# Optimization experiments

Measured on AMD Instinct MI355X. Metric: run time of the kernel, lower is better.

The kernel has to match this reference:

```python
import jax, jax.numpy as jnp
import numpy as np

NEG = -1e9      # stands in for -inf; exp(NEG)=0 in fp32 and is grad-safe
SK_TAU = 0.05   # sinkhorn temperature (module constant)


def _gconv(A, x, Wa, ba, Wu, bu):
    # Gconv: A <- F.normalize(A, p=1, dim=-2) (column-wise L1), then
    # out = A @ relu(a_fc(x)) + relu(u_fc(x))
    Anorm = A / jnp.maximum(jnp.sum(jnp.abs(A), axis=1, keepdims=True), 1e-12)
    ax = jax.nn.relu(x @ Wa + ba)
    ux = jax.nn.relu(x @ Wu + bu)
    return jnp.einsum('bnm,bmd->bnd', Anorm, ax) + ux


def _sinkhorn(s, n1, n2, max_iter, tau):
    # Masked, batched equivalent of the per-sample torch sinkhorn
    # (valid region [0:n1, 0:n2]; entries outside stay at NEG -> exp -> 0).
    # Assumes n1 <= n2 == N so no per-sample transpose branch triggers.
    B, N, M = s.shape
    row_ok = jnp.arange(N)[None, :, None] < n1[:, None, None]
    col_ok = jnp.arange(M)[None, None, :] < n2[:, None, None]
    mask = row_ok & col_ok
    log_s = jnp.where(mask, s / tau, NEG)
    for i in range(max_iter):
        axis = 2 if i % 2 == 0 else 1  # even: row-normalize, odd: col-normalize
        log_s = log_s - jax.scipy.special.logsumexp(log_s, axis=axis, keepdims=True)
        log_s = jnp.where(mask, log_s, NEG)
    return jnp.exp(log_s)


def _forward(feat1, feat2, A1, A2, n1, n2, sk_max_iter,
             W0a, b0a, W0u, b0u, W1a, b1a, W1u, b1u, Wc, bc, Aaff0, Aaff1):
    # gnn layer 0 (Siamese: same weights on both graphs)
    emb1 = _gconv(A1, feat1, W0a, b0a, W0u, b0u)
    emb2 = _gconv(A2, feat2, W0a, b0a, W0u, b0u)
    # i == gnn_layer-2: affinity -> sinkhorn -> cross-graph update
    s = jnp.einsum('bnd,de,bme->bnm', emb1, Aaff0, emb2)
    s = _sinkhorn(s, n1, n2, sk_max_iter, SK_TAU)
    new1 = jnp.concatenate([emb1, jnp.einsum('bnm,bmd->bnd', s, emb2)], axis=-1) @ Wc + bc
    new2 = jnp.concatenate([emb2, jnp.einsum('bnm,bnd->bmd', s, emb1)], axis=-1) @ Wc + bc
    emb1, emb2 = new1, new2
    # gnn layer 1 (final)
    emb1 = _gconv(A1, emb1, W1a, b1a, W1u, b1u)
    emb2 = _gconv(A2, emb2, W1a, b1a, W1u, b1u)
    s = jnp.einsum('bnd,de,bme->bnm', emb1, Aaff1, emb2)
    return _sinkhorn(s, n1, n2, sk_max_iter, SK_TAU)


def setup_inputs() -> dict:
    key = jax.random.key(0)
    B, N = 32, 256
    C_IN, C_HID, C_OUT = 1024, 2048, 2048
    ks = jax.random.split(key, 16)

    feat1 = jax.random.normal(ks[0], (B, N, C_IN), dtype=jnp.float32)
    feat2 = jax.random.normal(ks[1], (B, N, C_IN), dtype=jnp.float32)
    A1 = jax.random.uniform(ks[2], (B, N, N), dtype=jnp.float32)
    A2 = jax.random.uniform(ks[3], (B, N, N), dtype=jnp.float32)
    n1 = jax.random.randint(ks[4], (B,), N // 2, N + 1).astype(jnp.int32)
    n2 = jnp.full((B,), N, dtype=jnp.int32)

    def lin(k, fan_in, fan_out):
        stdv = 1.0 / np.sqrt(fan_in)
        kw, kb = jax.random.split(k)
        W = jax.random.uniform(kw, (fan_in, fan_out), minval=-stdv, maxval=stdv, dtype=jnp.float32)
        b = jax.random.uniform(kb, (fan_out,), minval=-stdv, maxval=stdv, dtype=jnp.float32)
        return W, b

    W0a, b0a = lin(ks[5], C_IN, C_HID)
    W0u, b0u = lin(ks[6], C_IN, C_HID)
    W1a, b1a = lin(ks[7], C_HID, C_OUT)
    W1u, b1u = lin(ks[8], C_HID, C_OUT)
    Wc, bc = lin(ks[9], 2 * C_HID, C_HID)
    # WeightedInnerProdAffinity: A ~ U(-1/sqrt(d), 1/sqrt(d)) + I
    Aaff0 = jax.random.uniform(ks[10], (C_HID, C_HID), minval=-1/np.sqrt(C_HID), maxval=1/np.sqrt(C_HID), dtype=jnp.float32) + jnp.eye(C_HID, dtype=jnp.float32)
    Aaff1 = jax.random.uniform(ks[11], (C_OUT, C_OUT), minval=-1/np.sqrt(C_OUT), maxval=1/np.sqrt(C_OUT), dtype=jnp.float32) + jnp.eye(C_OUT, dtype=jnp.float32)

    return {
        'feat1': feat1, 'feat2': feat2, 'A1': A1, 'A2': A2,
        'n1': n1, 'n2': n2, 'cross_iter_num': -1, 'sk_max_iter': 10,
        'W0a': W0a, 'b0a': b0a, 'W0u': W0u, 'b0u': b0u,
        'W1a': W1a, 'b1a': b1a, 'W1u': W1u, 'b1u': b1u,
        'Wc': Wc, 'bc': bc, 'Aaff0': Aaff0, 'Aaff1': Aaff1,
    }


def reference(feat1, feat2, A1, A2, n1, n2, cross_iter_num, sk_max_iter,
              W0a, b0a, W0u, b0u, W1a, b1a, W1u, b1u, Wc, bc, Aaff0, Aaff1):
    assert cross_iter_num <= 0  # PCA-GM path (IPCA-GM cross-iteration not exercised)
    return _forward(feat1, feat2, A1, A2, n1, n2, int(sk_max_iter),
                    W0a, b0a, W0u, b0u, W1a, b1a, W1u, b1u, Wc, bc, Aaff0, Aaff1)
```

## Files before the change

### kernel.cpp

```cpp
#include <hip/hip_runtime.h>
#include <math.h>

#define NEGV -1e9f
#define SK_TAU 0.05f

typedef __attribute__((ext_vector_type(4))) float f32x4;
typedef __attribute__((ext_vector_type(8))) short short8;

#define GLDS(g, l) __builtin_amdgcn_global_load_lds( \
    (const __attribute__((address_space(1))) void*)(g), \
    (__attribute__((address_space(3))) void*)(l), 16, 0, 0)

__device__ inline unsigned bf16rtn(float x) {
    unsigned u = __float_as_uint(x);
    return (u + 0x7FFFu + ((u >> 16) & 1u)) >> 16;
}
__device__ inline float bf2f(short h) {
    return __uint_as_float(((unsigned)(unsigned short)h) << 16);
}
__device__ inline void split1(float x, short& h, short& l) {
    unsigned hu = bf16rtn(x);
    h = (short)hu;
    float r = x - __uint_as_float(hu << 16);
    l = (short)(__float_as_uint(r) >> 16);
}
__device__ inline void cvt4(const float4 v, short4& h, short4& l) {
    unsigned h0 = bf16rtn(v.x), h1 = bf16rtn(v.y), h2 = bf16rtn(v.z), h3 = bf16rtn(v.w);
    h.x = (short)h0; h.y = (short)h1; h.z = (short)h2; h.w = (short)h3;
    float l0 = v.x - __uint_as_float(h0 << 16);
    float l1 = v.y - __uint_as_float(h1 << 16);
    float l2 = v.z - __uint_as_float(h2 << 16);
    float l3 = v.w - __uint_as_float(h3 << 16);
    l.x = (short)(__float_as_uint(l0) >> 16);
    l.y = (short)(__float_as_uint(l1) >> 16);
    l.z = (short)(__float_as_uint(l2) >> 16);
    l.w = (short)(__float_as_uint(l3) >> 16);
}
__device__ inline short8 pack8(const short4 a, const short4 b) {
    short8 r;
    r[0] = a.x; r[1] = a.y; r[2] = a.z; r[3] = a.w;
    r[4] = b.x; r[5] = b.y; r[6] = b.z; r[7] = b.w;
    return r;
}

__global__ __launch_bounds__(256) void colnorm_k(const float* __restrict__ A,
                                                 float* __restrict__ inv)
{
    int idx = blockIdx.x * 256 + threadIdx.x;
    int b = idx >> 8, m = idx & 255;
    const float* p = A + (long long)b * 65536 + m;
    float s = 0.f;
    #pragma unroll 8
    for (int n = 0; n < 256; ++n) s += fabsf(p[n * 256]);
    inv[idx] = 1.f / fmaxf(s, 1e-12f);
}

__global__ __launch_bounds__(256) void split_mat(const float* __restrict__ X,
                                                 short* __restrict__ H,
                                                 short* __restrict__ L, long long n4)
{
    long long i = (long long)blockIdx.x * 256 + threadIdx.x;
    long long stride = (long long)gridDim.x * 256;
    for (; i < n4; i += stride) {
        float4 v = ((const float4*)X)[i];
        short4 h, l;
        cvt4(v, h, l);
        ((short4*)H)[i] = h;
        ((short4*)L)[i] = l;
    }
}

template <int OM>
__global__ __launch_bounds__(256, 2) void gemm_w(
    const short* __restrict__ A1h, const short* __restrict__ A1l,
    const short* __restrict__ A2h, const short* __restrict__ A2l,
    int K1, int lda,
    const float* __restrict__ Bf, int K,
    float* __restrict__ Cf, short* __restrict__ Ch, short* __restrict__ Cl,
    const float* __restrict__ bias, int relu)
{
    __shared__ alignas(16) short lds[2][16384];

    const int tid = threadIdx.x;
    const int wave = tid >> 6, L = tid & 63;
    const int m0 = blockIdx.y * 128, n0 = blockIdx.x * 128;
    const int wm = (wave & 1) * 64, wn = (wave >> 1) * 64;
    const int lm = L & 15, lh = (L >> 4) * 8;
    const int c0 = wave * 2;

    long long grow[2];
    #pragma unroll
    for (int c = 0; c < 2; ++c)
        grow[c] = (long long)(m0 + (c0 + c) * 16 + lm) * lda + lh;

    const int bcol = tid & 127, bkh = tid >> 7;
    const float* bp = Bf + (long long)(bkh * 16) * 2048 + n0 + bcol;
    const int bws = (bcol >> 4) * 512 + (bcol & 15) * 8 + bkh * 256;

    f32x4 acc[4][4];
    #pragma unroll
    for (int i = 0; i < 4; ++i)
        #pragma unroll
        for (int j = 0; j < 4; ++j)
            acc[i][j] = (f32x4){0.f, 0.f, 0.f, 0.f};

    auto STAGE = [&](short* buf, int k0) {
        const short *sh, *sl;
        int ko;
        if (k0 < K1) { sh = A1h; sl = A1l; ko = k0; }
        else         { sh = A2h; sl = A2l; ko = k0 - K1; }
        #pragma unroll
        for (int c = 0; c < 2; ++c) {
            const int so = (c0 + c) * 512;
            GLDS(sh + grow[c] + ko, buf + so);
            GLDS(sl + grow[c] + ko, buf + 4096 + so);
        }
    };
    auto LOADB = [&](float br[16], int k0) {
        #pragma unroll
        for (int j = 0; j < 16; ++j)
            br[j] = bp[((long long)k0 + j) * 2048];
    };
    auto WRITEB = [&](short* buf, const float br[16]) {
        #pragma unroll
        for (int ks = 0; ks < 2; ++ks) {
            float4 v0 = {br[ks * 8 + 0], br[ks * 8 + 1], br[ks * 8 + 2], br[ks * 8 + 3]};
            float4 v1 = {br[ks * 8 + 4], br[ks * 8 + 5], br[ks * 8 + 6], br[ks * 8 + 7]};
            short4 h0, l0, h1, l1;
            cvt4(v0, h0, l0);
            cvt4(v1, h1, l1);
            *(short8*)(buf + 8192  + bws + ks * 128) = pack8(h0, h1);
            *(short8*)(buf + 12288 + bws + ks * 128) = pack8(l0, l1);
        }
    };

    const int ab = (wm >> 4) * 512 + L * 8;
    const int bb = (wn >> 4) * 512 + L * 8;
    auto COMPUTE = [&](const short* buf) {
        const short* AhS = buf;
        const short* AlS = buf + 4096;
        const short* BhS = buf + 8192;
        const short* BlS = buf + 12288;
        short8 AF[4], ALF[4], BFr[4], BLF[4];
        #pragma unroll
        for (int t = 0; t < 4; ++t) {
            AF[t]  = *(const short8*)(AhS + ab + t * 512);
            ALF[t] = *(const short8*)(AlS + ab + t * 512);
            BFr[t] = *(const short8*)(BhS + bb + t * 512);
            BLF[t] = *(const short8*)(BlS + bb + t * 512);
        }
        #pragma unroll
        for (int ti = 0; ti < 4; ++ti)
            #pragma unroll
            for (int tj = 0; tj < 4; ++tj) {
                acc[ti][tj] = __builtin_amdgcn_mfma_f32_16x16x32_bf16(AF[ti],  BFr[tj], acc[ti][tj], 0, 0, 0);
                acc[ti][tj] = __builtin_amdgcn_mfma_f32_16x16x32_bf16(AF[ti],  BLF[tj], acc[ti][tj], 0, 0, 0);
                acc[ti][tj] = __builtin_amdgcn_mfma_f32_16x16x32_bf16(ALF[ti], BFr[tj], acc[ti][tj], 0, 0, 0);
            }
    };

    const int NT = K >> 5;
    float brA[16], brB[16];

    LOADB(brA, 0);
    STAGE(lds[0], 0);
    LOADB(brB, 32);
    WRITEB(lds[0], brA);
    LOADB(brA, 64);

    for (int t = 0; t < NT; t += 2) {
        __syncthreads();
        {
            STAGE(lds[1], (t + 1) << 5);
            WRITEB(lds[1], brB);
        }
        if (t + 3 < NT) LOADB(brB, (t + 3) << 5);
        COMPUTE(lds[0]);

        __syncthreads();
        if (t + 2 < NT) {
            STAGE(lds[0], (t + 2) << 5);
            WRITEB(lds[0], brA);
        }
        if (t + 4 < NT) LOADB(brA, (t + 4) << 5);
        COMPUTE(lds[1]);
    }

    const int lcol = L & 15, lrow = (L >> 4) * 4;
    float bv[4];
    #pragma unroll
    for (int tj = 0; tj < 4; ++tj)
        bv[tj] = bias ? bias[n0 + wn + tj * 16 + lcol] : 0.f;

    #pragma unroll
    for (int ti = 0; ti < 4; ++ti) {
        #pragma unroll
        for (int r = 0; r < 4; ++r) {
            int gr = m0 + wm + ti * 16 + lrow + r;
            #pragma unroll
            for (int tj = 0; tj < 4; ++tj) {
                int gcol = n0 + wn + tj * 16 + lcol;
                float v = acc[ti][tj][r] + bv[tj];
                if (relu) v = fmaxf(v, 0.f);
                long long idx = (long long)gr * 2048 + gcol;
                if (OM == 0) {
                    Cf[idx] = v;
                } else {
                    short hh, ll;
                    split1(v, hh, ll);
                    Ch[idx] = hh;
                    Cl[idx] = ll;
                }
            }
        }
    }
}

template <bool TA, bool ACC>
__global__ __launch_bounds__(256, 2) void bgemm_m(
    const float* __restrict__ A,
    const short* __restrict__ Bh_, const short* __restrict__ Bl_,
    short* __restrict__ Ch, short* __restrict__ Cl,
    const float* __restrict__ colscale)
{
    __shared__ alignas(16) short lds[2][16384];

    const int tid = threadIdx.x;
    const int wave = tid >> 6, L = tid & 63;
    const int z = blockIdx.z;
    const int n0 = blockIdx.x * 128, m0 = blockIdx.y * 128;
    const int wm = (wave & 1) * 64, wn = (wave >> 1) * 64;
    const long long sB = 524288;
    const float* Az = A + (long long)z * 65536;
    const float* cs = colscale ? colscale + z * 256 : nullptr;

    const int arow = tid & 127, akh = tid >> 7;
    const int aws = (arow >> 4) * 512 + (arow & 15) * 8 + akh * 256;
    const int bws = aws;

    f32x4 acc[4][4];
    #pragma unroll
    for (int i = 0; i < 4; ++i)
        #pragma unroll
        for (int j = 0; j < 4; ++j)
            acc[i][j] = (f32x4){0.f, 0.f, 0.f, 0.f};

    float ar[16];
    short brh[16], brl[16];

    auto LOADA = [&](int k0) {
        #pragma unroll
        for (int j = 0; j < 16; ++j) {
            int kk = k0 + akh * 16 + j;
            float v;
            if (TA) v = Az[(long long)kk * 256 + m0 + arow];
            else    v = Az[(long long)(m0 + arow) * 256 + kk];
            if (!TA && cs) v *= cs[kk];
            ar[j] = v;
        }
    };
    auto LOADBB = [&](int k0) {
        #pragma unroll
        for (int j = 0; j < 16; ++j) {
            long long off = (long long)z * sB +
                            (long long)(k0 + akh * 16 + j) * 2048 + n0 + arow;
            brh[j] = Bh_[off];
            brl[j] = Bl_[off];
        }
    };
    auto WRITES = [&](short* buf) {
        #pragma unroll
        for (int ks = 0; ks < 2; ++ks) {
            float4 v0 = {ar[ks * 8 + 0], ar[ks * 8 + 1], ar[ks * 8 + 2], ar[ks * 8 + 3]};
            float4 v1 = {ar[ks * 8 + 4], ar[ks * 8 + 5], ar[ks * 8 + 6], ar[ks * 8 + 7]};
            short4 h0, l0, h1, l1;
            cvt4(v0, h0, l0);
            cvt4(v1, h1, l1);
            *(short8*)(buf + aws + ks * 128)        = pack8(h0, h1);
            *(short8*)(buf + 4096 + aws + ks * 128) = pack8(l0, l1);
        }
        #pragma unroll
        for (int ks = 0; ks < 2; ++ks) {
            short8 h, l;
            #pragma unroll
            for (int i = 0; i < 8; ++i) { h[i] = brh[ks * 8 + i]; l[i] = brl[ks * 8 + i]; }
            *(short8*)(buf + 8192  + bws + ks * 128) = h;
            *(short8*)(buf + 12288 + bws + ks * 128) = l;
        }
    };

    const int ab = (wm >> 4) * 512 + L * 8;
    const int bb = (wn >> 4) * 512 + L * 8;
    auto COMPUTE = [&](const short* buf) {
        const short* AhS = buf;
        const short* AlS = buf + 4096;
        const short* BhS = buf + 8192;
        const short* BlS = buf + 12288;
        short8 AF[4], ALF[4], BFr[4], BLF[4];
        #pragma unroll
        for (int t = 0; t < 4; ++t) {
            AF[t]  = *(const short8*)(AhS + ab + t * 512);
            ALF[t] = *(const short8*)(AlS + ab + t * 512);
            BFr[t] = *(const short8*)(BhS + bb + t * 512);
            BLF[t] = *(const short8*)(BlS + bb + t * 512);
        }
        #pragma unroll
        for (int ti = 0; ti < 4; ++ti)
            #pragma unroll
            for (int tj = 0; tj < 4; ++tj) {
                acc[ti][tj] = __builtin_amdgcn_mfma_f32_16x16x32_bf16(AF[ti],  BFr[tj], acc[ti][tj], 0, 0, 0);
                acc[ti][tj] = __builtin_amdgcn_mfma_f32_16x16x32_bf16(AF[ti],  BLF[tj], acc[ti][tj], 0, 0, 0);
                acc[ti][tj] = __builtin_amdgcn_mfma_f32_16x16x32_bf16(ALF[ti], BFr[tj], acc[ti][tj], 0, 0, 0);
            }
    };

    LOADA(0);
    LOADBB(0);
    #pragma unroll
    for (int t = 0; t < 8; ++t) {
        WRITES(lds[t & 1]);
        __syncthreads();
        if (t < 7) { LOADA((t + 1) * 32); LOADBB((t + 1) * 32); }
        COMPUTE(lds[t & 1]);
    }

    const int lcol = L & 15, lrow = (L >> 4) * 4;
    #pragma unroll
    for (int ti = 0; ti < 4; ++ti) {
        #pragma unroll
        for (int r = 0; r < 4; ++r) {
            int gr = m0 + wm + ti * 16 + lrow + r;
            long long base = (long long)z * sB + (long long)gr * 2048;
            #pragma unroll
            for (int tj = 0; tj < 4; ++tj) {
                int gcol = n0 + wn + tj * 16 + lcol;
                long long idx = base + gcol;
                float v = acc[ti][tj][r];
                if (ACC) v += bf2f(Ch[idx]) + bf2f(Cl[idx]);
                short hh, ll;
                split1(v, hh, ll);
                Ch[idx] = hh;
                Cl[idx] = ll;
            }
        }
    }
}

__global__ __launch_bounds__(256) void gemm_bt_f64(
    const float* __restrict__ A,
    const short* __restrict__ Bh_, const short* __restrict__ Bl_,
    float* __restrict__ C)
{
    __shared__ float As[16][65];
    __shared__ float Bs[16][65];

    const int K = 2048;
    int z = blockIdx.z;
    const float* Az = A + (long long)z * 524288;
    C += (long long)z * 65536;

    int n0 = blockIdx.x * 64;
    int m0 = blockIdx.y * 64;
    int tid = threadIdx.x;
    int tx = tid & 15;
    int ty = tid >> 4;

    double acc[4][4];
    #pragma unroll
    for (int i = 0; i < 4; ++i)
        #pragma unroll
        for (int j = 0; j < 4; ++j) acc[i][j] = 0.0;

    int r  = tid >> 2;
    int c4 = (tid & 3) * 4;

    for (int k0 = 0; k0 < K; k0 += 16) {
        {
            const float4 v = *(const float4*)(Az + (long long)(m0 + r) * K + k0 + c4);
            As[c4 + 0][r] = v.x; As[c4 + 1][r] = v.y;
            As[c4 + 2][r] = v.z; As[c4 + 3][r] = v.w;
        }
        {
            long long off = (long long)z * 524288 + (long long)(n0 + r) * K + k0 + c4;
            short4 h = *(const short4*)(Bh_ + off);
            short4 l = *(const short4*)(Bl_ + off);
            Bs[c4 + 0][r] = bf2f(h.x) + bf2f(l.x);
            Bs[c4 + 1][r] = bf2f(h.y) + bf2f(l.y);
            Bs[c4 + 2][r] = bf2f(h.z) + bf2f(l.z);
            Bs[c4 + 3][r] = bf2f(h.w) + bf2f(l.w);
        }
        __syncthreads();

        #pragma unroll
        for (int kk = 0; kk < 16; ++kk) {
            double a[4], b[4];
            #pragma unroll
            for (int i = 0; i < 4; ++i) a[i] = (double)As[kk][ty + 16 * i];
            #pragma unroll
            for (int j = 0; j < 4; ++j) b[j] = (double)Bs[kk][tx + 16 * j];
            #pragma unroll
            for (int i = 0; i < 4; ++i)
                #pragma unroll
                for (int j = 0; j < 4; ++j)
                    acc[i][j] = fma(a[i], b[j], acc[i][j]);
        }
        __syncthreads();
    }

    #pragma unroll
    for (int i = 0; i < 4; ++i) {
        int rowl = m0 + ty + 16 * i;
        #pragma unroll
        for (int j = 0; j < 4; ++j)
            C[(long long)rowl * 256 + n0 + tx + 16 * j] = (float)acc[i][j];
    }
}

__global__ __launch_bounds__(1024, 4) void sk_fused(float* __restrict__ S,
                                                    const int* __restrict__ n1)
{
    __shared__ float pmax[16][256];
    __shared__ float psum[16][256];
    __shared__ float lseS[256];

    const int b = blockIdx.x;
    const int tid = threadIdx.x;
    const int w = tid >> 6, l = tid & 63;
    const int lim = n1[b];
    float* Sb = S + (long long)b * 65536;

    float4 v[16];
    #pragma unroll
    for (int r = 0; r < 16; ++r) {
        int n = w * 16 + r;
        if (n < lim) {
            float4 x = *(const float4*)(Sb + n * 256 + l * 4);
            v[r].x = x.x / SK_TAU; v[r].y = x.y / SK_TAU;
            v[r].z = x.z / SK_TAU; v[r].w = x.w / SK_TAU;
        } else {
            v[r] = (float4){NEGV, NEGV, NEGV, NEGV};
        }
    }

    for (int it = 0; it < 10; ++it) {
        if ((it & 1) == 0) {
            #pragma unroll
            for (int r = 0; r < 16; ++r) {
                if (w * 16 + r >= lim) continue;
                float m = fmaxf(fmaxf(v[r].x, v[r].y), fmaxf(v[r].z, v[r].w));
                #pragma unroll
                for (int off = 1; off < 64; off <<= 1) m = fmaxf(m, __shfl_xor(m, off));
                float s = expf(v[r].x - m) + expf(v[r].y - m) +
                          expf(v[r].z - m) + expf(v[r].w - m);
                #pragma unroll
                for (int off = 1; off < 64; off <<= 1) s += __shfl_xor(s, off);
                float lse = m + logf(s);
                v[r].x -= lse; v[r].y -= lse; v[r].z -= lse; v[r].w -= lse;
            }
        } else {
            float cm[4] = {-3.4e38f, -3.4e38f, -3.4e38f, -3.4e38f};
            #pragma unroll
            for (int r = 0; r < 16; ++r) {
                cm[0] = fmaxf(cm[0], v[r].x); cm[1] = fmaxf(cm[1], v[r].y);
                cm[2] = fmaxf(cm[2], v[r].z); cm[3] = fmaxf(cm[3], v[r].w);
            }
            float cs[4] = {0.f, 0.f, 0.f, 0.f};
            #pragma unroll
            for (int r = 0; r < 16; ++r) {
                cs[0] += expf(v[r].x - cm[0]); cs[1] += expf(v[r].y - cm[1]);
                cs[2] += expf(v[r].z - cm[2]); cs[3] += expf(v[r].w - cm[3]);
            }
            #pragma unroll
            for (int j = 0; j < 4; ++j) {
                pmax[w][l * 4 + j] = cm[j];
                psum[w][l * 4 + j] = cs[j];
            }
            __syncthreads();
            if (tid < 256) {
                float m = -3.4e38f, s = 0.f;
                #pragma unroll
                for (int ww = 0; ww < 16; ++ww) {
                    float pm = pmax[ww][tid], ps = psum[ww][tid];
                    float nm = fmaxf(m, pm);
                    s = s * expf(m - nm) + ps * expf(pm - nm);
                    m = nm;
                }
                lseS[tid] = m + logf(s);
            }
            __syncthreads();
            float l0 = lseS[l * 4 + 0], l1 = lseS[l * 4 + 1];
            float l2 = lseS[l * 4 + 2], l3 = lseS[l * 4 + 3];
            #pragma unroll
            for (int r = 0; r < 16; ++r) {
                if (w * 16 + r >= lim) continue;
                v[r].x -= l0; v[r].y -= l1; v[r].z -= l2; v[r].w -= l3;
            }
        }
    }

    #pragma unroll
    for (int r = 0; r < 16; ++r) {
        int n = w * 16 + r;
        float4 o;
        if (n < lim) {
            o.x = expf(v[r].x); o.y = expf(v[r].y);
            o.z = expf(v[r].z); o.w = expf(v[r].w);
        } else {
            o = (float4){0.f, 0.f, 0.f, 0.f};
        }
        *(float4*)(Sb + n * 256 + l * 4) = o;
    }
}

static void gw(hipStream_t st, int om, const short* Ah, const short* Al, int lda,
               const float* Bf, int K,
               float* Cf, short* Ch, short* Cl, const float* bias, int relu)
{
    dim3 grid(16, 64), block(256);
    if (om == 0)
        gemm_w<0><<<grid, block, 0, st>>>(Ah, Al, Ah, Al, K, lda, Bf, K,
                                          Cf, nullptr, nullptr, bias, relu);
    else
        gemm_w<1><<<grid, block, 0, st>>>(Ah, Al, Ah, Al, K, lda, Bf, K,
                                          nullptr, Ch, Cl, bias, relu);
}

static void gwcat(hipStream_t st, const short* A1h, const short* A1l,
                  const short* A2h, const short* A2l,
                  const float* Bf, short* Ch, short* Cl, const float* bias)
{
    dim3 grid(16, 64), block(256);
    gemm_w<1><<<grid, block, 0, st>>>(A1h, A1l, A2h, A2l, 2048, 2048, Bf, 4096,
                                      nullptr, Ch, Cl, bias, 0);
}

extern "C" void kernel_launch(void* const* d_in, const int* in_sizes, int n_in,
                              void* d_out, int out_size, void* d_ws, size_t ws_size,
                              hipStream_t stream)
{
    const float* feat1 = (const float*)d_in[0];
    const float* feat2 = (const float*)d_in[1];
    const float* A1    = (const float*)d_in[2];
    const float* A2    = (const float*)d_in[3];
    const int*   n1    = (const int*)d_in[4];
    const float* W0a = (const float*)d_in[8];  const float* b0a = (const float*)d_in[9];
    const float* W0u = (const float*)d_in[10]; const float* b0u = (const float*)d_in[11];
    const float* W1a = (const float*)d_in[12]; const float* b1a = (const float*)d_in[13];
    const float* W1u = (const float*)d_in[14]; const float* b1u = (const float*)d_in[15];
    const float* Wc  = (const float*)d_in[16]; const float* bc  = (const float*)d_in[17];
    const float* Aaff0 = (const float*)d_in[18];
    const float* Aaff1 = (const float*)d_in[19];

    const long long TSZ = 16777216LL;
    const long long PL  = 16777216LL;
    const long long PF  = 8388608LL;

    float* T1f = (float*)d_ws;
    float* T2f = T1f + TSZ;
    float* T3f = T2f + TSZ;
    float* T4f = T3f + TSZ;
    short *T1h = (short*)T1f, *T1l = T1h + PL;
    short *T2h = (short*)T2f, *T2l = T2h + PL;
    short *T3h = (short*)T3f, *T3l = T3h + PL;
    short *T4h = (short*)T4f, *T4l = T4h + PL;

    short* f1h = (short*)T4f;      short* f1l = f1h + PF;
    short* f2h = f1h + 2 * PF;     short* f2l = f1h + 3 * PF;
    float* invA = (float*)T4f;
    float* invB = invA + 8192;

    float* S    = (float*)d_out;
    float* inv1 = S;
    float* inv2 = S + 8192;

    dim3 bgrid(16, 2, 32), bblk(256);

    split_mat<<<2048, 256, 0, stream>>>(feat1, f1h, f1l, 8192LL * 1024 / 4);
    split_mat<<<2048, 256, 0, stream>>>(feat2, f2h, f2l, 8192LL * 1024 / 4);

    gw(stream, 1, f1h, f1l, 1024, W0u, 1024, nullptr, T1h, T1l, b0u, 1);
    gw(stream, 1, f2h, f2l, 1024, W0u, 1024, nullptr, T2h, T2l, b0u, 1);
    gw(stream, 1, f1h, f1l, 1024, W0a, 1024, nullptr, T3h, T3l, b0a, 1);
    colnorm_k<<<32, 256, 0, stream>>>(A1, invA);
    colnorm_k<<<32, 256, 0, stream>>>(A2, invB);
    bgemm_m<false, true><<<bgrid, bblk, 0, stream>>>(A1, T3h, T3l, T1h, T1l, invA);
    gw(stream, 1, f2h, f2l, 1024, W0a, 1024, nullptr, T3h, T3l, b0a, 1);
    bgemm_m<false, true><<<bgrid, bblk, 0, stream>>>(A2, T3h, T3l, T2h, T2l, invB);

    gw(stream, 0, T1h, T1l, 2048, Aaff0, 2048, T3f, nullptr, nullptr, nullptr, 0);
    gemm_bt_f64<<<dim3(4, 4, 32), 256, 0, stream>>>(T3f, T2h, T2l, S);

    sk_fused<<<32, 1024, 0, stream>>>(S, n1);

    bgemm_m<false, false><<<bgrid, bblk, 0, stream>>>(S, T2h, T2l, T3h, T3l, nullptr);
    gwcat(stream, T1h, T1l, T3h, T3l, Wc, T4h, T4l, bc);
    bgemm_m<true, false><<<bgrid, bblk, 0, stream>>>(S, T1h, T1l, T3h, T3l, nullptr);
    gwcat(stream, T2h, T2l, T3h, T3l, Wc, T1h, T1l, bc);

    gw(stream, 1, T4h, T4l, 2048, W1a, 2048, nullptr, T2h, T2l, b1a, 1);
    gw(stream, 1, T4h, T4l, 2048, W1u, 2048, nullptr, T3h, T3l, b1u, 1);
    colnorm_k<<<32, 256, 0, stream>>>(A1, inv1);
    bgemm_m<false, true><<<bgrid, bblk, 0, stream>>>(A1, T2h, T2l, T3h, T3l, inv1);
    gw(stream, 1, T1h, T1l, 2048, W1a, 2048, nullptr, T2h, T2l, b1a, 1);
    gw(stream, 1, T1h, T1l, 2048, W1u, 2048, nullptr, T4h, T4l, b1u, 1);
    colnorm_k<<<32, 256, 0, stream>>>(A2, inv2);
    bgemm_m<false, true><<<bgrid, bblk, 0, stream>>>(A2, T2h, T2l, T4h, T4l, inv2);

    gw(stream, 0, T3h, T3l, 2048, Aaff1, 2048, T1f, nullptr, nullptr, nullptr, 0);
    gemm_bt_f64<<<dim3(4, 4, 32), 256, 0, stream>>>(T1f, T4h, T4l, S);

    sk_fused<<<32, 1024, 0, stream>>>(S, n1);
}
```

Before: 4.340 ms.

## Enlarge weight GEMM to 256x256 tiles with 8 waves and phased MFMA schedule

```diff
diff --git a/kernel.cpp b/kernel.cpp
--- a/kernel.cpp
+++ b/kernel.cpp
@@ -71,7 +71,7 @@
 }
 
 template <int OM>
-__global__ __launch_bounds__(256, 2) void gemm_w(
+__global__ __launch_bounds__(512, 2) void gemm_w8(
     const short* __restrict__ A1h, const short* __restrict__ A1l,
     const short* __restrict__ A2h, const short* __restrict__ A2l,
     int K1, int lda,
@@ -79,12 +79,12 @@
     float* __restrict__ Cf, short* __restrict__ Ch, short* __restrict__ Cl,
     const float* __restrict__ bias, int relu)
 {
-    __shared__ alignas(16) short lds[2][16384];
+    extern __shared__ short lds_s[];
 
     const int tid = threadIdx.x;
     const int wave = tid >> 6, L = tid & 63;
-    const int m0 = blockIdx.y * 128, n0 = blockIdx.x * 128;
-    const int wm = (wave & 1) * 64, wn = (wave >> 1) * 64;
+    const int m0 = blockIdx.y * 256, n0 = blockIdx.x * 256;
+    const int wm = (wave & 1) * 128, wn = (wave >> 1) * 64;
     const int lm = L & 15, lh = (L >> 4) * 8;
     const int c0 = wave * 2;
 
@@ -93,98 +93,107 @@
     for (int c = 0; c < 2; ++c)
         grow[c] = (long long)(m0 + (c0 + c) * 16 + lm) * lda + lh;
 
-    const int bcol = tid & 127, bkh = tid >> 7;
+    const int bcol = tid & 255, bkh = tid >> 8;
     const float* bp = Bf + (long long)(bkh * 16) * 2048 + n0 + bcol;
     const int bws = (bcol >> 4) * 512 + (bcol & 15) * 8 + bkh * 256;
 
-    f32x4 acc[4][4];
-    #pragma unroll
-    for (int i = 0; i < 4; ++i)
+    f32x4 acc[8][4];
+    #pragma unroll
+    for (int i = 0; i < 8; ++i)
         #pragma unroll
         for (int j = 0; j < 4; ++j)
             acc[i][j] = (f32x4){0.f, 0.f, 0.f, 0.f};
 
-    auto STAGE = [&](short* buf, int k0) {
-        const short *sh, *sl;
-        int ko;
-        if (k0 < K1) { sh = A1h; sl = A1l; ko = k0; }
-        else         { sh = A2h; sl = A2l; ko = k0 - K1; }
-        #pragma unroll
-        for (int c = 0; c < 2; ++c) {
-            const int so = (c0 + c) * 512;
-            GLDS(sh + grow[c] + ko, buf + so);
-            GLDS(sl + grow[c] + ko, buf + 4096 + so);
-        }
+    float brA[16];
+    short8 AF[4], ALF[4], BFr[4], BLF[4];
+    const int abase = (wm >> 4) * 512 + L * 8;
+    const int bbase = (wn >> 4) * 512 + L * 8;
+
+    auto GLDS_A = [&](short* buf, int k0, int plane) {
+        const short* s; int ko;
+        if (k0 < K1) { s = plane ? A1l : A1h; ko = k0; }
+        else         { s = plane ? A2l : A2h; ko = k0 - K1; }
+        #pragma unroll
+        for (int c = 0; c < 2; ++c)
+            GLDS(s + grow[c] + ko, buf + plane * 8192 + (c0 + c) * 512);
     };
-    auto LOADB = [&](float br[16], int k0) {
+    auto LOADB = [&](int k0) {
         #pragma unroll
         for (int j = 0; j < 16; ++j)
-            br[j] = bp[((long long)k0 + j) * 2048];
+            brA[j] = bp[((long long)k0 + j) * 2048];
     };
-    auto WRITEB = [&](short* buf, const float br[16]) {
+    auto WRITEB = [&](short* buf) {
         #pragma unroll
         for (int ks = 0; ks < 2; ++ks) {
-            float4 v0 = {br[ks * 8 + 0], br[ks * 8 + 1], br[ks * 8 + 2], br[ks * 8 + 3]};
-            float4 v1 = {br[ks * 8 + 4], br[ks * 8 + 5], br[ks * 8 + 6], br[ks * 8 + 7]};
+            float4 v0 = {brA[ks * 8 + 0], brA[ks * 8 + 1], brA[ks * 8 + 2], brA[ks * 8 + 3]};
+            float4 v1 = {brA[ks * 8 + 4], brA[ks * 8 + 5], brA[ks * 8 + 6], brA[ks * 8 + 7]};
             short4 h0, l0, h1, l1;
             cvt4(v0, h0, l0);
             cvt4(v1, h1, l1);
-            *(short8*)(buf + 8192  + bws + ks * 128) = pack8(h0, h1);
-            *(short8*)(buf + 12288 + bws + ks * 128) = pack8(l0, l1);
+            *(short8*)(buf + 16384 + bws + ks * 128) = pack8(h0, h1);
+            *(short8*)(buf + 24576 + bws + ks * 128) = pack8(l0, l1);
         }
     };
 
-    const int ab = (wm >> 4) * 512 + L * 8;
-    const int bb = (wn >> 4) * 512 + L * 8;
-    auto COMPUTE = [&](const short* buf) {
-        const short* AhS = buf;
-        const short* AlS = buf + 4096;
-        const short* BhS = buf + 8192;
-        const short* BlS = buf + 12288;
-        short8 AF[4], ALF[4], BFr[4], BLF[4];
-        #pragma unroll
-        for (int t = 0; t < 4; ++t) {
-            AF[t]  = *(const short8*)(AhS + ab + t * 512);
-            ALF[t] = *(const short8*)(AlS + ab + t * 512);
-            BFr[t] = *(const short8*)(BhS + bb + t * 512);
-            BLF[t] = *(const short8*)(BlS + bb + t * 512);
-        }
-        #pragma unroll
-        for (int ti = 0; ti < 4; ++ti)
-            #pragma unroll
-            for (int tj = 0; tj < 4; ++tj) {
-                acc[ti][tj] = __builtin_amdgcn_mfma_f32_16x16x32_bf16(AF[ti],  BFr[tj], acc[ti][tj], 0, 0, 0);
-                acc[ti][tj] = __builtin_amdgcn_mfma_f32_16x16x32_bf16(AF[ti],  BLF[tj], acc[ti][tj], 0, 0, 0);
-                acc[ti][tj] = __builtin_amdgcn_mfma_f32_16x16x32_bf16(ALF[ti], BFr[tj], acc[ti][tj], 0, 0, 0);
-            }
-    };
+#define RD_A8(H) do { _Pragma("unroll") for (int i_ = 0; i_ < 4; ++i_) { \
+        AF[i_]  = *(const short8*)(cur + abase + ((H) * 4 + i_) * 512); \
+        ALF[i_] = *(const short8*)(cur + 8192 + abase + ((H) * 4 + i_) * 512); } } while (0)
+
+#define RD_B8(NH) do { _Pragma("unroll") for (int j_ = 0; j_ < 2; ++j_) { \
+        BFr[(NH) * 2 + j_] = *(const short8*)(cur + 16384 + bbase + ((NH) * 2 + j_) * 512); \
+        BLF[(NH) * 2 + j_] = *(const short8*)(cur + 24576 + bbase + ((NH) * 2 + j_) * 512); } } while (0)
+
+#define MQ8(MH, NH) do { _Pragma("unroll") for (int i_ = 0; i_ < 4; ++i_) \
+        _Pragma("unroll") for (int j_ = 0; j_ < 2; ++j_) { \
+            acc[(MH)*4+i_][(NH)*2+j_] = __builtin_amdgcn_mfma_f32_16x16x32_bf16(AF[i_],  BFr[(NH)*2+j_], acc[(MH)*4+i_][(NH)*2+j_], 0, 0, 0); \
+            acc[(MH)*4+i_][(NH)*2+j_] = __builtin_amdgcn_mfma_f32_16x16x32_bf16(AF[i_],  BLF[(NH)*2+j_], acc[(MH)*4+i_][(NH)*2+j_], 0, 0, 0); \
+            acc[(MH)*4+i_][(NH)*2+j_] = __builtin_amdgcn_mfma_f32_16x16x32_bf16(ALF[i_], BFr[(NH)*2+j_], acc[(MH)*4+i_][(NH)*2+j_], 0, 0, 0); } } while (0)
+
+#define PH_IN() do { __builtin_amdgcn_s_barrier(); \
+        asm volatile("s_waitcnt lgkmcnt(0)" ::: "memory"); \
+        __builtin_amdgcn_sched_barrier(0); \
+        __builtin_amdgcn_s_setprio(1); } while (0)
+#define PH_OUT() do { __builtin_amdgcn_s_setprio(0); \
+        __builtin_amdgcn_s_barrier(); } while (0)
 
     const int NT = K >> 5;
-    float brA[16], brB[16];
-
-    LOADB(brA, 0);
-    STAGE(lds[0], 0);
-    LOADB(brB, 32);
-    WRITEB(lds[0], brA);
-    LOADB(brA, 64);
-
-    for (int t = 0; t < NT; t += 2) {
-        __syncthreads();
-        {
-            STAGE(lds[1], (t + 1) << 5);
-            WRITEB(lds[1], brB);
-        }
-        if (t + 3 < NT) LOADB(brB, (t + 3) << 5);
-        COMPUTE(lds[0]);
-
-        __syncthreads();
-        if (t + 2 < NT) {
-            STAGE(lds[0], (t + 2) << 5);
-            WRITEB(lds[0], brA);
-        }
-        if (t + 4 < NT) LOADB(brA, (t + 4) << 5);
-        COMPUTE(lds[1]);
-    }
+
+    LOADB(0);
+    GLDS_A(lds_s, 0, 0);
+    GLDS_A(lds_s, 0, 1);
+    WRITEB(lds_s);
+    __syncthreads();
+
+    for (int t = 0; t < NT; ++t) {
+        short* cur = lds_s + (t & 1) * 32768;
+        short* nxt = lds_s + ((t + 1) & 1) * 32768;
+        const bool more = (t + 1) < NT;
+        const int kn = (t + 1) << 5;
+
+        RD_A8(0); RD_B8(0);
+        if (more) { LOADB(kn); GLDS_A(nxt, kn, 0); }
+        PH_IN(); MQ8(0, 0); PH_OUT();
+
+        RD_B8(1);
+        if (more) GLDS_A(nxt, kn, 1);
+        PH_IN(); MQ8(0, 1); PH_OUT();
+
+        RD_A8(1);
+        if (more) WRITEB(nxt);
+        PH_IN(); MQ8(1, 0); PH_OUT();
+
+        __builtin_amdgcn_s_setprio(1);
+        MQ8(1, 1);
+        __builtin_amdgcn_s_setprio(0);
+        asm volatile("s_waitcnt vmcnt(0)" ::: "memory");
+        __builtin_amdgcn_s_barrier();
+    }
+
+#undef RD_A8
+#undef RD_B8
+#undef MQ8
+#undef PH_IN
+#undef PH_OUT
 
     const int lcol = L & 15, lrow = (L >> 4) * 4;
     float bv[4];
@@ -193,7 +202,7 @@
         bv[tj] = bias ? bias[n0 + wn + tj * 16 + lcol] : 0.f;
 
     #pragma unroll
-    for (int ti = 0; ti < 4; ++ti) {
+    for (int ti = 0; ti < 8; ++ti) {
         #pragma unroll
         for (int r = 0; r < 4; ++r) {
             int gr = m0 + wm + ti * 16 + lrow + r;
@@ -512,26 +521,38 @@
     }
 }
 
+static void set_lds_attr() {
+    static bool done = false;
+    if (done) return;
+    hipFuncSetAttribute((const void*)gemm_w8<0>,
+                        hipFuncAttributeMaxDynamicSharedMemorySize, 131072);
+    hipFuncSetAttribute((const void*)gemm_w8<1>,
+                        hipFuncAttributeMaxDynamicSharedMemorySize, 131072);
+    done = true;
+}
+
 static void gw(hipStream_t st, int om, const short* Ah, const short* Al, int lda,
                const float* Bf, int K,
                float* Cf, short* Ch, short* Cl, const float* bias, int relu)
 {
-    dim3 grid(16, 64), block(256);
+    set_lds_attr();
+    dim3 grid(8, 32), block(512);
     if (om == 0)
-        gemm_w<0><<<grid, block, 0, st>>>(Ah, Al, Ah, Al, K, lda, Bf, K,
-                                          Cf, nullptr, nullptr, bias, relu);
+        gemm_w8<0><<<grid, block, 131072, st>>>(Ah, Al, Ah, Al, K, lda, Bf, K,
+                                                Cf, nullptr, nullptr, bias, relu);
     else
-        gemm_w<1><<<grid, block, 0, st>>>(Ah, Al, Ah, Al, K, lda, Bf, K,
-                                          nullptr, Ch, Cl, bias, relu);
+        gemm_w8<1><<<grid, block, 131072, st>>>(Ah, Al, Ah, Al, K, lda, Bf, K,
+                                                nullptr, Ch, Cl, bias, relu);
 }
 
 static void gwcat(hipStream_t st, const short* A1h, const short* A1l,
                   const short* A2h, const short* A2l,
                   const float* Bf, short* Ch, short* Cl, const float* bias)
 {
-    dim3 grid(16, 64), block(256);
-    gemm_w<1><<<grid, block, 0, st>>>(A1h, A1l, A2h, A2l, 2048, 2048, Bf, 4096,
-                                      nullptr, Ch, Cl, bias, 0);
+    set_lds_attr();
+    dim3 grid(8, 32), block(512);
+    gemm_w8<1><<<grid, block, 131072, st>>>(A1h, A1l, A2h, A2l, 2048, 2048, Bf, 4096,
+                                            nullptr, Ch, Cl, bias, 0);
 }
 
 extern "C" void kernel_launch(void* const* d_in, const int* in_sizes, int n_in,
```

Result: no change. 4.276 ms (-1.5%).
